# Optimization experiments

Hardware: AMD Instinct MI355X
Metric: run time of the kernel (lower is better)

The kernel has to match this reference:

```python
import math
import jax, jax.numpy as jnp
import numpy as np

HIDDEN = 2048
N_HEAD = 16
HEAD_DIM = HIDDEN // N_HEAD
LAYER_NUMBER = 1  # max(1, layer_number)
NORM_FACTOR = math.sqrt(HEAD_DIM) * LAYER_NUMBER


def build_alibi(seq_len, n_head):
    # n_head is a power of 2 -> slopes_i = 2^(-8*(i+1)/n_head)  (ALiBi paper)
    slopes = 2.0 ** (-8.0 * jnp.arange(1, n_head + 1, dtype=jnp.float32) / n_head)
    pos = jnp.arange(seq_len, dtype=jnp.float32)
    return slopes[:, None, None] * pos[None, None, :]  # (n_head, 1, seq_len)


def setup_inputs() -> dict:
    key = jax.random.key(0)
    ks = jax.random.split(key, 6)
    B, S = 2, 2048
    hidden_states = jax.random.normal(ks[0], (B, S, HIDDEN), jnp.float32)
    residual = jax.random.normal(ks[1], (B, S, HIDDEN), jnp.float32)
    attention_mask = jnp.ones((B, S), jnp.float32)  # no padding
    W_qkv = jax.random.normal(ks[2], (3 * HIDDEN, HIDDEN), jnp.float32) * (1.0 / math.sqrt(HIDDEN))
    b_qkv = jax.random.normal(ks[3], (3 * HIDDEN,), jnp.float32) * 0.02
    W_dense = jax.random.normal(ks[4], (HIDDEN, HIDDEN), jnp.float32) * (1.0 / math.sqrt(HIDDEN))
    b_dense = jax.random.normal(ks[5], (HIDDEN,), jnp.float32) * 0.02
    return {"hidden_states": hidden_states, "residual": residual,
            "attention_mask": attention_mask, "W_qkv": W_qkv, "b_qkv": b_qkv,
            "W_dense": W_dense, "b_dense": b_dense}


def reference(hidden_states, residual, attention_mask, W_qkv, b_qkv, W_dense, b_dense):
    B, S, H = hidden_states.shape
    nh, hd = N_HEAD, HEAD_DIM

    # fused QKV projection; split_tensor_along_last_dim over the per-head 3*hd axis
    mixed = hidden_states @ W_qkv.T + b_qkv              # [B,S,3H]
    mixed = mixed.reshape(B, S, nh, 3, hd)
    q = mixed[..., 0, :]                                  # [B,S,nh,hd]
    k = mixed[..., 1, :]
    v = mixed[..., 2, :]

    # baddbmm: beta*alibi + alpha*(q @ k^T)
    alibi = build_alibi(S, nh)                            # (nh,1,S)
    beta = 1.0 / LAYER_NUMBER
    alpha = 1.0 / NORM_FACTOR
    scores = alpha * jnp.einsum('bqnd,bknd->bnqk', q, k) + beta * alibi[None]  # [B,nh,S,S]

    # BloomScaledSoftmax: scale by layer_number, apply padded causal mask,
    # softmax in fp32, zero out masked probs
    scores = scores * LAYER_NUMBER
    mask_bool = attention_mask == 0.0                     # [B,S] True where padded
    causal = jnp.tril(jnp.ones((S, S), dtype=bool))       # [S,S]
    padded = (mask_bool[:, None, :, None]                 # query side
              | (~causal)[None, None]                     # causal
              | mask_bool[:, None, None, :])              # key side -> [B,1,S,S]
    scores = jnp.where(padded, jnp.float32(-10000.0), scores)
    probs = jax.nn.softmax(scores.astype(jnp.float32), axis=-1) * (~padded)
    probs = probs.astype(v.dtype)

    # attention_dropout/hidden_dropout are identity in eval mode
    context = jnp.einsum('bnqk,bknd->bqnd', probs, v).reshape(B, S, H)
    out = context @ W_dense.T + b_dense                   # dense (skip_bias_add folded)
    return residual + out
```

## Files before the change

kernel.cpp:

```cpp
#include <hip/hip_runtime.h>
#include <math.h>

#define HIDDEN 2048
#define NHEAD 16
#define HD 128
#define SEQ 2048
#define BATCH 2
#define MROWS (BATCH * SEQ)
#define K3 (3 * HIDDEN)

#define SCORE_SCALE 0.08838834764831845f

using short8 = __attribute__((ext_vector_type(8))) short;
using f32x4 = __attribute__((ext_vector_type(4))) float;

__device__ __forceinline__ unsigned short f2bf(float f) {
  union { float f; unsigned int u; } v; v.f = f;
  const unsigned int u = v.u;
  return (unsigned short)((u + 0x7FFFu + ((u >> 16) & 1u)) >> 16);
}

__device__ __forceinline__ void gl2lds16(const void* g, void* l) {
#pragma clang diagnostic push
#pragma clang diagnostic ignored "-Waddress-space-conversion"
  __builtin_amdgcn_global_load_lds(
      (const __attribute__((address_space(1))) unsigned int*)g,
      (__attribute__((address_space(3))) unsigned int*)l, 16, 0, 0);
#pragma clang diagnostic pop
}

__global__ __launch_bounds__(256) void cvt_all(
    const float* __restrict__ s0, unsigned short* __restrict__ d0, int n0,
    const float* __restrict__ s1, unsigned short* __restrict__ d1, int n1,
    const float* __restrict__ s2, unsigned short* __restrict__ d2, int n2) {
  int i = (blockIdx.x * 256 + threadIdx.x) * 8;
  const float* src;
  unsigned short* dst;
  if (i < n0) {
    src = s0; dst = d0;
  } else if (i < n0 + n1) {
    src = s1; dst = d1; i -= n0;
  } else {
    src = s2; dst = d2; i -= n0 + n1;
    if (i >= n2) return;
  }
  const float4 a = *(const float4*)(src + i);
  const float4 b = *(const float4*)(src + i + 4);
  ushort4 oa, ob;
  oa.x = f2bf(a.x); oa.y = f2bf(a.y); oa.z = f2bf(a.z); oa.w = f2bf(a.w);
  ob.x = f2bf(b.x); ob.y = f2bf(b.y); ob.z = f2bf(b.z); ob.w = f2bf(b.w);
  *(ushort4*)(dst + i) = oa;
  *(ushort4*)(dst + i + 4) = ob;
}

template <int MODE>
__global__ __launch_bounds__(256) void gemm_mfma(
    const unsigned short* __restrict__ A, const unsigned short* __restrict__ W,
    const float* __restrict__ bias, const float* __restrict__ residual,
    unsigned short* __restrict__ q, unsigned short* __restrict__ k,
    unsigned short* __restrict__ v, float* __restrict__ outf, int K) {
  __shared__ __align__(16) unsigned short As[128 * 32];
  __shared__ __align__(16) unsigned short Bs[128 * 32];
  const int tid = threadIdx.x;
  const int lane = tid & 63;
  const int wave = tid >> 6;
  const int l15 = lane & 15;
  const int quad = lane >> 4;
  const int wr = wave >> 1, wc = wave & 1;
  const int m0 = blockIdx.y << 7;
  const int n0 = blockIdx.x << 7;

  f32x4 acc[4][4];
#pragma unroll
  for (int i = 0; i < 4; ++i)
#pragma unroll
    for (int j = 0; j < 4; ++j) {
      f32x4 z = {0.f, 0.f, 0.f, 0.f};
      acc[i][j] = z;
    }

  const int kg0 = tid >> 7, mr0 = tid & 127;
  const int kg1 = (tid + 256) >> 7, mr1 = tid & 127;

  for (int k0 = 0; k0 < K; k0 += 32) {
    gl2lds16(A + (size_t)(m0 + mr0) * K + k0 + kg0 * 8, (char*)As + tid * 16);
    gl2lds16(W + (size_t)(n0 + mr0) * K + k0 + kg0 * 8, (char*)Bs + tid * 16);
    gl2lds16(A + (size_t)(m0 + mr1) * K + k0 + kg1 * 8,
             (char*)As + 4096 + tid * 16);
    gl2lds16(W + (size_t)(n0 + mr1) * K + k0 + kg1 * 8,
             (char*)Bs + 4096 + tid * 16);
    __syncthreads();
    short8 af[4], bf[4];
#pragma unroll
    for (int i = 0; i < 4; ++i)
      af[i] = *(const short8*)((const char*)As + quad * 2048 +
                               (wr * 64 + i * 16 + l15) * 16);
#pragma unroll
    for (int j = 0; j < 4; ++j)
      bf[j] = *(const short8*)((const char*)Bs + quad * 2048 +
                               (wc * 64 + j * 16 + l15) * 16);
#pragma unroll
    for (int i = 0; i < 4; ++i)
#pragma unroll
      for (int j = 0; j < 4; ++j)
        acc[i][j] =
            __builtin_amdgcn_mfma_f32_16x16x32_bf16(af[i], bf[j], acc[i][j],
                                                    0, 0, 0);
    __syncthreads();
  }

  if (MODE == 0) {
#pragma unroll
    for (int i = 0; i < 4; ++i) {
#pragma unroll
      for (int j = 0; j < 4; ++j) {
        const int n = n0 + wc * 64 + j * 16 + l15;
        const float bi = bias[n];
        const int h = n / 384;
        const int rem = n - h * 384;
        const int which = rem >> 7;
        const int d = rem & 127;
        const int mb = m0 + wr * 64 + i * 16 + quad * 4;
        const int bb = mb >> 11, ssb = mb & 2047;
        const int bh = (bb << 4) + h;
        if (which == 2) {
          const int dt = d >> 4, dl = d & 15;
          const int ksup = ssb >> 5, ntl = (ssb >> 4) & 1, qq = (ssb >> 2) & 3;
          ushort4 pk;
          pk.x = f2bf(acc[i][j][0] + bi);
          pk.y = f2bf(acc[i][j][1] + bi);
          pk.z = f2bf(acc[i][j][2] + bi);
          pk.w = f2bf(acc[i][j][3] + bi);
          *(ushort4*)(v +
                      ((((size_t)(bh * 8 + dt) * (SEQ / 32) + ksup) * 4 + qq) *
                       16 + dl) * 8 + ntl * 4) = pk;
        } else {
          unsigned short* dst = (which == 0) ? q : k;
#pragma unroll
          for (int p = 0; p < 4; ++p)
            dst[((size_t)(bh << 11) + ssb + p) * HD + d] =
                f2bf(acc[i][j][p] + bi);
        }
      }
    }
  } else {
#pragma unroll
    for (int i = 0; i < 4; ++i) {
#pragma unroll
      for (int j = 0; j < 4; ++j) {
        const int n = n0 + wc * 64 + j * 16 + l15;
        const float bi = bias[n];
#pragma unroll
        for (int p = 0; p < 4; ++p) {
          const int m = m0 + wr * 64 + i * 16 + quad * 4 + p;
          outf[(size_t)m * HIDDEN + n] =
              acc[i][j][p] + bi + residual[(size_t)m * HIDDEN + n];
        }
      }
    }
  }
}

__global__ __launch_bounds__(256) void attn_mfma3(
    const unsigned short* __restrict__ qb, const unsigned short* __restrict__ kb,
    const unsigned short* __restrict__ vt4, unsigned short* __restrict__ ctx) {
  __shared__ __align__(16) unsigned short Ks[8192];
  __shared__ __align__(16) unsigned short Vs[8192];

  const int tid = threadIdx.x;
  const int lane = tid & 63;
  const int w = tid >> 6;
  const int l15 = lane & 15;
  const int quad = lane >> 4;
  const int bt = gridDim.x - 1 - blockIdx.x;
  const int q0 = bt << 6;
  const int h = blockIdx.y, b = blockIdx.z;
  const int bh = b * NHEAD + h;
  const float slope = exp2f(-0.5f * (float)(h + 1));
  const unsigned short* qp = qb + ((size_t)bh * SEQ + q0 + w * 16) * HD;
  const unsigned short* kp = kb + (size_t)bh * SEQ * HD;
  const unsigned short* vp = vt4 + (size_t)bh * SEQ * HD;

  short8 qf[4];
#pragma unroll
  for (int dt = 0; dt < 4; ++dt)
    qf[dt] = *(const short8*)(qp + (size_t)l15 * HD + dt * 32 + quad * 8);

  f32x4 O[8];
#pragma unroll
  for (int i = 0; i < 8; ++i) {
    f32x4 z = {0.f, 0.f, 0.f, 0.f};
    O[i] = z;
  }
  float mrow = -3.0e38f, lrow = 0.f;
  const int qg = q0 + w * 16 + l15;

  for (int kt = 0; kt <= bt; ++kt) {
#pragma unroll
    for (int p = 0; p < 4; ++p) {
      const int idx = tid + p * 256;
      const int reg = idx >> 6;
      const int nts = reg >> 2, dts = reg & 3;
      const int qs = (idx >> 4) & 3, ls = idx & 15;
      gl2lds16(kp + (size_t)(kt * 64 + nts * 16 + ls) * HD + dts * 32 + qs * 8,
               (char*)Ks + idx * 16);
    }
#pragma unroll
    for (int p = 0; p < 4; ++p) {
      const int idx = tid + p * 256;
      const int ntv = idx >> 7, off = idx & 127;
      gl2lds16(vp + ((size_t)(ntv * 64 + kt * 2)) * 512 + off * 8,
               (char*)Vs + idx * 16);
    }
    __syncthreads();

    f32x4 sc[4];
#pragma unroll
    for (int nt = 0; nt < 4; ++nt) {
      f32x4 z = {0.f, 0.f, 0.f, 0.f};
      sc[nt] = z;
    }
    const int ntmax = (kt == bt) ? (w + 1) : 4;
#pragma unroll
    for (int dt = 0; dt < 4; ++dt) {
#pragma unroll
      for (int nt = 0; nt < 4; ++nt) {
        if (nt < ntmax) {
          const short8 kf = *(const short8*)(
              (const char*)Ks + ((((nt * 4 + dt) * 4 + quad) * 16 + l15) << 4));
          sc[nt] = __builtin_amdgcn_mfma_f32_16x16x32_bf16(kf, qf[dt], sc[nt],
                                                           0, 0, 0);
        }
      }
    }

    const bool diag = (kt == bt);
    float pv[4][4];
    float pm = -3.0e38f;
#pragma unroll
    for (int nt = 0; nt < 4; ++nt) {
      const int kbase = kt * 64 + nt * 16 + quad * 4;
#pragma unroll
      for (int r = 0; r < 4; ++r) {
        const int kg = kbase + r;
        float s = fmaf(sc[nt][r], SCORE_SCALE, slope * (float)kg);
        if (diag && kg > qg) s = -1.0e30f;
        pv[nt][r] = s;
        pm = fmaxf(pm, s);
      }
    }
    pm = fmaxf(pm, __shfl_xor(pm, 16, 64));
    pm = fmaxf(pm, __shfl_xor(pm, 32, 64));
    const float mnew = fmaxf(mrow, pm);
    const float alpha = __expf(mrow - mnew);
    mrow = mnew;
    float rsum = 0.f;
#pragma unroll
    for (int nt = 0; nt < 4; ++nt)
#pragma unroll
      for (int r = 0; r < 4; ++r) {
        const float p = __expf(pv[nt][r] - mnew);
        pv[nt][r] = p;
        rsum += p;
      }
    rsum += __shfl_xor(rsum, 16, 64);
    rsum += __shfl_xor(rsum, 32, 64);
    lrow = lrow * alpha + rsum;

    float aO[4];
#pragma unroll
    for (int r = 0; r < 4; ++r)
      aO[r] = __shfl(alpha, (quad << 4) + (quad << 2) + r, 64);
#pragma unroll
    for (int o = 0; o < 8; ++o)
#pragma unroll
      for (int r = 0; r < 4; ++r) O[o][r] *= aO[r];

    union { short8 s; unsigned int u[4]; } pf[2];
#pragma unroll
    for (int nt = 0; nt < 4; ++nt) {
      const unsigned int lo =
          (unsigned int)f2bf(pv[nt][0]) | ((unsigned int)f2bf(pv[nt][1]) << 16);
      const unsigned int hi =
          (unsigned int)f2bf(pv[nt][2]) | ((unsigned int)f2bf(pv[nt][3]) << 16);
      pf[nt >> 1].u[(nt & 1) * 2] = lo;
      pf[nt >> 1].u[(nt & 1) * 2 + 1] = hi;
    }

#pragma unroll
    for (int s2 = 0; s2 < 2; ++s2) {
#pragma unroll
      for (int nt = 0; nt < 8; ++nt) {
        const short8 vf = *(const short8*)(
            (const char*)Vs + nt * 2048 + s2 * 1024 + quad * 256 + l15 * 16);
        O[nt] = __builtin_amdgcn_mfma_f32_16x16x32_bf16(pf[s2].s, vf, O[nt],
                                                        0, 0, 0);
      }
    }
    __syncthreads();
  }

  const float linv = 1.f / lrow;
  float iO[4];
#pragma unroll
  for (int r = 0; r < 4; ++r)
    iO[r] = __shfl(linv, (quad << 4) + (quad << 2) + r, 64);
#pragma unroll
  for (int nt = 0; nt < 8; ++nt)
#pragma unroll
    for (int r = 0; r < 4; ++r)
      ctx[((size_t)b * SEQ + q0 + w * 16 + quad * 4 + r) * HIDDEN + h * HD +
          nt * 16 + l15] = f2bf(O[nt][r] * iO[r]);
}

extern "C" void kernel_launch(void* const* d_in, const int* in_sizes, int n_in,
                              void* d_out, int out_size, void* d_ws,
                              size_t ws_size, hipStream_t stream) {
  const float* hs = (const float*)d_in[0];
  const float* res = (const float*)d_in[1];
  const float* Wqkv = (const float*)d_in[3];
  const float* bqkv = (const float*)d_in[4];
  const float* Wd = (const float*)d_in[5];
  const float* bd = (const float*)d_in[6];
  float* out = (float*)d_out;

  const size_t per = (size_t)BATCH * NHEAD * SEQ * HD;
  const size_t n_hs = (size_t)MROWS * HIDDEN;
  const size_t n_wq = (size_t)K3 * HIDDEN;
  const size_t n_wd = (size_t)HIDDEN * HIDDEN;

  unsigned short* ws = (unsigned short*)d_ws;
  unsigned short* qb = ws;
  unsigned short* kb = qb + per;
  unsigned short* vtb = kb + per;
  unsigned short* ctxb = vtb + per;
  unsigned short* hs_bf = ctxb + n_hs;
  unsigned short* wq_bf = hs_bf + n_hs;
  unsigned short* wd_bf = wq_bf + n_wq;

  dim3 blk(256);
  const unsigned cvt_blocks = (unsigned)((n_hs + n_wq + n_wd) / 8 / 256);
  cvt_all<<<dim3(cvt_blocks), blk, 0, stream>>>(
      hs, hs_bf, (int)n_hs, Wqkv, wq_bf, (int)n_wq, Wd, wd_bf, (int)n_wd);
  gemm_mfma<0><<<dim3(K3 / 128, MROWS / 128), blk, 0, stream>>>(
      hs_bf, wq_bf, bqkv, nullptr, qb, kb, vtb, nullptr, HIDDEN);
  attn_mfma3<<<dim3(SEQ / 64, NHEAD, BATCH), blk, 0, stream>>>(qb, kb, vtb,
                                                               ctxb);
  gemm_mfma<1><<<dim3(HIDDEN / 128, MROWS / 128), blk, 0, stream>>>(
      ctxb, wd_bf, bd, res, nullptr, nullptr, nullptr, out, HIDDEN);
}
```

Before: 602.7 us.

## Replace GEMMs with 256-row double-buffered LDS tiles, swizzled grid, and prefetch

Both linear-projection GEMMs move from a 128x128 tile with 256 threads to a 256-row tile with 512 threads (256 or 128 output columns), a K-step of 64, and double-buffered LDS. The next K-tile is prefetched while MFMAs run, and an XCD-style block swizzle remaps the grid. Wave priority is raised around the MFMA bursts. The aim is higher data reuse per LDS load and load/compute overlap. In exchange the kernel uses more registers and LDS and launches fewer blocks, especially for the dense GEMM.

```diff
diff --git a/kernel.cpp b/kernel.cpp
--- a/kernel.cpp
+++ b/kernel.cpp
@@ -53,84 +53,129 @@
   *(ushort4*)(dst + i + 4) = ob;
 }
 
-template <int MODE>
-__global__ __launch_bounds__(256) void gemm_mfma(
+template <int MODE, int BROWS>
+__global__ __launch_bounds__(512) void gemm256(
     const unsigned short* __restrict__ A, const unsigned short* __restrict__ W,
     const float* __restrict__ bias, const float* __restrict__ residual,
     unsigned short* __restrict__ q, unsigned short* __restrict__ k,
-    unsigned short* __restrict__ v, float* __restrict__ outf, int K) {
-  __shared__ __align__(16) unsigned short As[128 * 32];
-  __shared__ __align__(16) unsigned short Bs[128 * 32];
+    unsigned short* __restrict__ v, float* __restrict__ outf) {
+  constexpr int K = HIDDEN;
+  constexpr int NT = K / 64;
+  constexpr int NB = BROWS / 64;
+  constexpr int BTB = BROWS * 128;
+  __shared__ __align__(16) unsigned short L[(65536 + 2 * BTB) / 2];
+
   const int tid = threadIdx.x;
   const int lane = tid & 63;
+  const int l15 = lane & 15;
+  const int quad = (lane >> 4) & 3;
   const int wave = tid >> 6;
-  const int l15 = lane & 15;
-  const int quad = lane >> 4;
-  const int wr = wave >> 1, wc = wave & 1;
-  const int m0 = blockIdx.y << 7;
-  const int n0 = blockIdx.x << 7;
-
-  f32x4 acc[4][4];
-#pragma unroll
-  for (int i = 0; i < 4; ++i)
-#pragma unroll
-    for (int j = 0; j < 4; ++j) {
+  const int wr = wave >> 2;
+  const int wc = wave & 3;
+
+  const int gx = gridDim.x;
+  const int nwg = gx * gridDim.y;
+  const int flat = blockIdx.y * gx + blockIdx.x;
+  const int swz = (flat & 7) * (nwg >> 3) + (flat >> 3);
+  const int bx = swz % gx, by = swz / gx;
+  const int n0 = bx * BROWS;
+  const int m0 = by << 8;
+
+  f32x4 acc[8][NB];
+#pragma unroll
+  for (int i = 0; i < 8; ++i)
+#pragma unroll
+    for (int j = 0; j < NB; ++j) {
       f32x4 z = {0.f, 0.f, 0.f, 0.f};
       acc[i][j] = z;
     }
 
-  const int kg0 = tid >> 7, mr0 = tid & 127;
-  const int kg1 = (tid + 256) >> 7, mr1 = tid & 127;
-
-  for (int k0 = 0; k0 < K; k0 += 32) {
-    gl2lds16(A + (size_t)(m0 + mr0) * K + k0 + kg0 * 8, (char*)As + tid * 16);
-    gl2lds16(W + (size_t)(n0 + mr0) * K + k0 + kg0 * 8, (char*)Bs + tid * 16);
-    gl2lds16(A + (size_t)(m0 + mr1) * K + k0 + kg1 * 8,
-             (char*)As + 4096 + tid * 16);
-    gl2lds16(W + (size_t)(n0 + mr1) * K + k0 + kg1 * 8,
-             (char*)Bs + 4096 + tid * 16);
+  auto stageA = [&](const int t, const int buf) {
+#pragma unroll
+    for (int p = 0; p < 4; ++p) {
+      const int idx = tid + p * 512;
+      gl2lds16(A + (size_t)(m0 + (idx & 255)) * K + t * 64 + (idx >> 8) * 8,
+               (char*)L + buf * 32768 + idx * 16);
+    }
+  };
+  auto stageB = [&](const int t, const int buf) {
+#pragma unroll
+    for (int p = 0; p < NB; ++p) {
+      const int idx = tid + p * 512;
+      gl2lds16(W + (size_t)(n0 + (idx & (BROWS - 1))) * K + t * 64 +
+                   (idx / BROWS) * 8,
+               (char*)L + 65536 + buf * BTB + idx * 16);
+    }
+  };
+
+  auto ktile = [&](const int cur, const int t) {
+    const char* lA = (const char*)L + cur * 32768;
+    const char* lB = (const char*)L + 65536 + cur * BTB;
+    const bool pf = (t + 1) < NT;
+    short8 bf[NB];
+#pragma unroll
+    for (int kk = 0; kk < 2; ++kk) {
+#pragma unroll
+      for (int mh = 0; mh < 2; ++mh) {
+        if (kk == 0 && mh == 0 && pf) stageA(t + 1, cur ^ 1);
+        if (kk == 0 && mh == 1 && pf) stageB(t + 1, cur ^ 1);
+        if (mh == 0) {
+#pragma unroll
+          for (int j = 0; j < NB; ++j)
+            bf[j] = *(const short8*)(
+                lB + (((kk * 4 + quad) * BROWS + wc * (BROWS / 4) + j * 16 +
+                       l15) << 4));
+        }
+        short8 af[4];
+#pragma unroll
+        for (int i = 0; i < 4; ++i)
+          af[i] = *(const short8*)(
+              lA + (((kk * 4 + quad) * 256 + wr * 128 + (mh * 4 + i) * 16 +
+                     l15) << 4));
+        __builtin_amdgcn_s_setprio(1);
+#pragma unroll
+        for (int i = 0; i < 4; ++i)
+#pragma unroll
+          for (int j = 0; j < NB; ++j)
+            acc[mh * 4 + i][j] = __builtin_amdgcn_mfma_f32_16x16x32_bf16(
+                af[i], bf[j], acc[mh * 4 + i][j], 0, 0, 0);
+        __builtin_amdgcn_s_setprio(0);
+        if (!(kk == 1 && mh == 1)) __builtin_amdgcn_s_barrier();
+      }
+    }
     __syncthreads();
-    short8 af[4], bf[4];
-#pragma unroll
-    for (int i = 0; i < 4; ++i)
-      af[i] = *(const short8*)((const char*)As + quad * 2048 +
-                               (wr * 64 + i * 16 + l15) * 16);
-#pragma unroll
-    for (int j = 0; j < 4; ++j)
-      bf[j] = *(const short8*)((const char*)Bs + quad * 2048 +
-                               (wc * 64 + j * 16 + l15) * 16);
-#pragma unroll
-    for (int i = 0; i < 4; ++i)
-#pragma unroll
-      for (int j = 0; j < 4; ++j)
-        acc[i][j] =
-            __builtin_amdgcn_mfma_f32_16x16x32_bf16(af[i], bf[j], acc[i][j],
-                                                    0, 0, 0);
-    __syncthreads();
+  };
+
+  stageA(0, 0);
+  stageB(0, 0);
+  __syncthreads();
+  for (int t = 0; t < NT; t += 2) {
+    ktile(0, t);
+    ktile(1, t + 1);
   }
 
   if (MODE == 0) {
 #pragma unroll
-    for (int i = 0; i < 4; ++i) {
-#pragma unroll
-      for (int j = 0; j < 4; ++j) {
-        const int n = n0 + wc * 64 + j * 16 + l15;
+    for (int mi = 0; mi < 8; ++mi) {
+#pragma unroll
+      for (int nj = 0; nj < NB; ++nj) {
+        const int n = n0 + wc * (BROWS / 4) + nj * 16 + l15;
         const float bi = bias[n];
         const int h = n / 384;
         const int rem = n - h * 384;
         const int which = rem >> 7;
         const int d = rem & 127;
-        const int mb = m0 + wr * 64 + i * 16 + quad * 4;
+        const int mb = m0 + wr * 128 + mi * 16 + quad * 4;
         const int bb = mb >> 11, ssb = mb & 2047;
         const int bh = (bb << 4) + h;
         if (which == 2) {
           const int dt = d >> 4, dl = d & 15;
           const int ksup = ssb >> 5, ntl = (ssb >> 4) & 1, qq = (ssb >> 2) & 3;
           ushort4 pk;
-          pk.x = f2bf(acc[i][j][0] + bi);
-          pk.y = f2bf(acc[i][j][1] + bi);
-          pk.z = f2bf(acc[i][j][2] + bi);
-          pk.w = f2bf(acc[i][j][3] + bi);
+          pk.x = f2bf(acc[mi][nj][0] + bi);
+          pk.y = f2bf(acc[mi][nj][1] + bi);
+          pk.z = f2bf(acc[mi][nj][2] + bi);
+          pk.w = f2bf(acc[mi][nj][3] + bi);
           *(ushort4*)(v +
                       ((((size_t)(bh * 8 + dt) * (SEQ / 32) + ksup) * 4 + qq) *
                        16 + dl) * 8 + ntl * 4) = pk;
@@ -139,22 +184,22 @@
 #pragma unroll
           for (int p = 0; p < 4; ++p)
             dst[((size_t)(bh << 11) + ssb + p) * HD + d] =
-                f2bf(acc[i][j][p] + bi);
+                f2bf(acc[mi][nj][p] + bi);
         }
       }
     }
   } else {
 #pragma unroll
-    for (int i = 0; i < 4; ++i) {
-#pragma unroll
-      for (int j = 0; j < 4; ++j) {
-        const int n = n0 + wc * 64 + j * 16 + l15;
+    for (int mi = 0; mi < 8; ++mi) {
+#pragma unroll
+      for (int nj = 0; nj < NB; ++nj) {
+        const int n = n0 + wc * (BROWS / 4) + nj * 16 + l15;
         const float bi = bias[n];
 #pragma unroll
         for (int p = 0; p < 4; ++p) {
-          const int m = m0 + wr * 64 + i * 16 + quad * 4 + p;
+          const int m = m0 + wr * 128 + mi * 16 + quad * 4 + p;
           outf[(size_t)m * HIDDEN + n] =
-              acc[i][j][p] + bi + residual[(size_t)m * HIDDEN + n];
+              acc[mi][nj][p] + bi + residual[(size_t)m * HIDDEN + n];
         }
       }
     }
@@ -342,10 +387,10 @@
   const unsigned cvt_blocks = (unsigned)((n_hs + n_wq + n_wd) / 8 / 256);
   cvt_all<<<dim3(cvt_blocks), blk, 0, stream>>>(
       hs, hs_bf, (int)n_hs, Wqkv, wq_bf, (int)n_wq, Wd, wd_bf, (int)n_wd);
-  gemm_mfma<0><<<dim3(K3 / 128, MROWS / 128), blk, 0, stream>>>(
-      hs_bf, wq_bf, bqkv, nullptr, qb, kb, vtb, nullptr, HIDDEN);
+  gemm256<0, 256><<<dim3(K3 / 256, MROWS / 256), dim3(512), 0, stream>>>(
+      hs_bf, wq_bf, bqkv, nullptr, qb, kb, vtb, nullptr);
   attn_mfma3<<<dim3(SEQ / 64, NHEAD, BATCH), blk, 0, stream>>>(qb, kb, vtb,
                                                                ctxb);
-  gemm_mfma<1><<<dim3(HIDDEN / 128, MROWS / 128), blk, 0, stream>>>(
-      ctxb, wd_bf, bd, res, nullptr, nullptr, nullptr, out, HIDDEN);
-}
+  gemm256<1, 128><<<dim3(HIDDEN / 128, MROWS / 256), dim3(512), 0, stream>>>(
+      ctxb, wd_bf, bd, res, nullptr, nullptr, nullptr, out);
+}
```

Result: faster. 561.7 us (-6.8%).
